# Kernel tuning notes

Hardware: AMD Instinct MI355X
Metric: run time of the kernel (lower is better)

## Reference

```python
import jax, jax.numpy as jnp
import numpy as np
from jax import lax

EPS = 1e-5

def setup_inputs() -> dict:
    key = jax.random.key(0)
    ks = jax.random.split(key, 8)
    B, D, H, W = 2, 96, 96, 96
    K, N, R = 4, 16, 6
    return {
        "x": jax.random.normal(ks[0], (B, D, H, W), jnp.float32),
        "x_proj_weight": jax.random.normal(ks[1], (K, R + 2 * N, D), jnp.float32) * 0.05,
        "dt_projs_weight": jax.random.normal(ks[2], (K, D, R), jnp.float32) * 0.05,
        "dt_projs_bias": jax.random.normal(ks[3], (K, D), jnp.float32) * 0.05,
        "A_logs": jax.random.uniform(ks[4], (K * D, N), jnp.float32, 0.0, 1.0),
        "Ds": jax.random.normal(ks[5], (K * D,), jnp.float32) * 0.1,
        "norm_weight": jnp.ones((D,), jnp.float32),
        "norm_bias": jnp.zeros((D,), jnp.float32),
    }

def _cross_scan(x):
    # x: [B,C,H,W] -> xs: [B,4,C,L]; dirs: row-major, col-major, and their flips
    B, C, H, W = x.shape
    x_hw = x.reshape(B, C, H * W)
    x_wh = jnp.swapaxes(x, 2, 3).reshape(B, C, H * W)
    return jnp.stack([x_hw, x_wh, x_hw[..., ::-1], x_wh[..., ::-1]], axis=1)

def _cross_merge(ys, H, W):
    # ys: [B,4,C,L] -> y: [B,C,L]
    B, K, C, L = ys.shape
    ys = ys[:, 0:2] + ys[:, 2:4][..., ::-1]
    y_wh = jnp.swapaxes(ys[:, 1].reshape(B, C, W, H), 2, 3).reshape(B, C, L)
    return ys[:, 0] + y_wh

def _forward(x, x_proj_weight, dt_projs_weight, dt_projs_bias, A_logs, Ds,
             norm_weight, norm_bias):
    B, D, H, W = x.shape
    L = H * W
    K, _, R = dt_projs_weight.shape
    N = A_logs.shape[1]

    xs = _cross_scan(x)                                        # [B,K,D,L]
    x_dbl = jnp.einsum('bkdl,kcd->bkcl', xs, x_proj_weight)    # [B,K,R+2N,L]
    dts, Bs, Cs = x_dbl[:, :, :R], x_dbl[:, :, R:R + N], x_dbl[:, :, R + N:]
    dts = jnp.einsum('bkrl,kdr->bkdl', dts, dt_projs_weight)   # [B,K,D,L]

    A = -jnp.exp(A_logs).reshape(K, D, N)                      # [K,D,N]
    delta = jax.nn.softplus(dts + dt_projs_bias[None, :, :, None])  # [B,K,D,L]

    # time-major for scan
    u_t = jnp.moveaxis(xs, 3, 0)       # [L,B,K,D]
    d_t = jnp.moveaxis(delta, 3, 0)    # [L,B,K,D]
    B_t = jnp.moveaxis(Bs, 3, 0)       # [L,B,K,N]
    C_t = jnp.moveaxis(Cs, 3, 0)       # [L,B,K,N]

    def step(h, inp):
        u, dlt, b, c = inp
        h = jnp.exp(dlt[..., None] * A) * h + (dlt * u)[..., None] * b[:, :, None, :]
        y = jnp.einsum('bkdn,bkn->bkd', h, c)
        return h, y

    h0 = jnp.zeros((B, K, D, N), xs.dtype)
    _, ys = lax.scan(step, h0, (u_t, d_t, B_t, C_t))           # ys: [L,B,K,D]
    ys = jnp.moveaxis(ys, 0, 3)                                # [B,K,D,L]
    ys = ys + Ds.reshape(1, K, D, 1) * xs                      # skip term

    y = _cross_merge(ys, H, W)                                 # [B,D,L]
    y = jnp.swapaxes(y, 1, 2)                                  # [B,L,D]
    # out_norm: LayerNorm over channel dim
    mu = y.mean(-1, keepdims=True)
    var = y.var(-1, keepdims=True)
    y = (y - mu) / jnp.sqrt(var + EPS) * norm_weight + norm_bias
    return y.reshape(B, H, W, D)

def reference(x, x_proj_weight, dt_projs_weight, dt_projs_bias, A_logs, Ds,
              norm_weight, norm_bias):
    return _forward(x, x_proj_weight, dt_projs_weight, dt_projs_bias,
                    A_logs, Ds, norm_weight, norm_bias)
```

## Files before the change

### kernel.cpp

```cpp
#include <hip/hip_runtime.h>
#include <hip/hip_bf16.h>
#include <hip/hip_fp16.h>


constexpr int Bn = 2, Kn = 4, Dn = 96, Hn = 96, Wn = 96, Ln = Hn * Wn;
constexpr int Nn = 16, Rn = 6;
constexpr int CCn = 192, CLn = 48;

#define DI __device__ __forceinline__

DI float bf2f(unsigned short u) { return __uint_as_float(((unsigned)u) << 16); }
DI bool probe_bf16(const void* nw) { return ((const unsigned*)nw)[0] == 0x3F803F80u; }
DI float ld_in(const void* p, long i, bool bf) {
  return bf ? bf2f(((const unsigned short*)p)[i]) : ((const float*)p)[i];
}
DI float fexp2(float x) {
#if __has_builtin(__builtin_amdgcn_exp2f)
  return __builtin_amdgcn_exp2f(x);
#else
  return exp2f(x);
#endif
}
DI float softplus_fast(float v) {
  return (v > 15.f) ? v : __logf(1.f + __expf(v));
}
constexpr float LOG2E = 1.44269504088896340736f;

__global__ __launch_bounds__(256) void k_convert(
    const void* __restrict__ xpw, const void* __restrict__ dtw,
    const void* __restrict__ dtb, const void* __restrict__ Al,
    const void* __restrict__ Ds, const void* __restrict__ nw,
    const void* __restrict__ nb,
    float* __restrict__ wp_f, float* __restrict__ wdt_f,
    float* __restrict__ bias_f, float* __restrict__ Al_f,
    float* __restrict__ dsum, float* __restrict__ nw_f, float* __restrict__ nb_f) {
  bool bf = probe_bf16(nw);
  int gtid = blockIdx.x * 256 + threadIdx.x;
  int gs = gridDim.x * 256;
  for (int i = gtid; i < Kn * 38 * Dn; i += gs) wp_f[i] = ld_in(xpw, i, bf);
  for (int i = gtid; i < Kn * Dn * Rn; i += gs) wdt_f[i] = ld_in(dtw, i, bf);
  for (int i = gtid; i < Kn * Dn; i += gs) bias_f[i] = ld_in(dtb, i, bf);
  for (int i = gtid; i < Kn * Dn * Nn; i += gs)
    Al_f[i] = -__expf(ld_in(Al, i, bf)) * LOG2E;
  for (int i = gtid; i < Dn; i += gs) {
    dsum[i] = ld_in(Ds, i, bf) + ld_in(Ds, 96 + i, bf) +
              ld_in(Ds, 192 + i, bf) + ld_in(Ds, 288 + i, bf);
    nw_f[i] = ld_in(nw, i, bf);
    nb_f[i] = ld_in(nb, i, bf);
  }
}

__global__ __launch_bounds__(256) void k_xl(const void* __restrict__ x,
                                            const void* __restrict__ nwraw,
                                            float* __restrict__ xl) {
  __shared__ float tile[96 * 97];
  bool bf = probe_bf16(nwraw);
  int l0 = blockIdx.x * 96, b = blockIdx.y;
  long srcbase = (long)b * Dn * Ln;
  for (int i = threadIdx.x; i < 96 * 96; i += 256) {
    int d = i / 96, j = i - d * 96;
    tile[d * 97 + j] = ld_in(x, srcbase + (long)d * Ln + l0 + j, bf);
  }
  __syncthreads();
  float* dst = xl + ((size_t)b * Ln + l0) * 96;
  for (int i = threadIdx.x; i < 96 * 96; i += 256) {
    int j = i / 96, d = i - j * 96;
    dst[(size_t)j * 96 + d] = tile[d * 97 + j];
  }
}

__global__ __launch_bounds__(256) void k_perm(const float* __restrict__ xl,
                                              float* __restrict__ xlT) {
  int m0 = blockIdx.x * 96, b = blockIdx.y;
  int w = blockIdx.x;
  const float* src = xl + (size_t)b * Ln * 96;
  float* dst = xlT + (size_t)b * Ln * 96;
  for (int i = threadIdx.x; i < 96 * 24; i += 256) {
    int r = i / 24, q = i - r * 24;
    *(float4*)(dst + (size_t)(m0 + r) * 96 + q * 4) =
        *(const float4*)(src + (size_t)(r * 96 + w) * 96 + q * 4);
  }
}

__global__ __launch_bounds__(256) void k_proj(
    const float* __restrict__ xl, const float* __restrict__ xlT,
    const float* __restrict__ wp_f, const float* __restrict__ wdt_f,
    const float* __restrict__ bias_f,
    __half2* __restrict__ ddu, float* __restrict__ BCg) {
  constexpr int TL = 64;
  __shared__ __half xt[TL * 102];
  __shared__ float wp[40 * 100];
  __shared__ float xd[40 * 70];
  __shared__ float wdt[96 * 6];
  __shared__ float bias[96];
  int tile = blockIdx.x, k = blockIdx.y, b = blockIdx.z;
  int l0 = tile * TL;
  int tid = threadIdx.x;
  bool rev = (k & 2) != 0;

  for (int i = tid; i < 40 * 100; i += 256) {
    int c = i / 100, dd = i - c * 100;
    wp[i] = (c < 38 && dd < 96) ? wp_f[k * 38 * 96 + c * 96 + dd] : 0.f;
  }
  for (int i = tid; i < 96 * 6; i += 256) wdt[i] = wdt_f[k * 96 * 6 + i];
  if (tid < 96) bias[tid] = bias_f[k * 96 + tid];
  {
    const float* xsrc = ((k & 1) ? xlT : xl) + (size_t)b * Ln * 96;
    for (int i = tid; i < TL * 24; i += 256) {
      int r = i / 24, q = i - r * 24;
      int g = rev ? (Ln - 1 - l0 - r) : (l0 + r);
      float4 v = *(const float4*)(xsrc + (size_t)g * 96 + q * 4);
      *(__half2*)(&xt[r * 102 + q * 4]) = __floats2half2_rn(v.x, v.y);
      *(__half2*)(&xt[r * 102 + q * 4 + 2]) = __floats2half2_rn(v.z, v.w);
    }
  }
  __syncthreads();

  {
    int jg = tid & 31, cg = tid >> 5;
    int j0 = jg * 2, c0 = cg * 5;
    float acc[5][2];
#pragma unroll
    for (int i = 0; i < 5; ++i) { acc[i][0] = 0.f; acc[i][1] = 0.f; }
    for (int dd = 0; dd < 96; dd += 4) {
      float xv[2][4];
#pragma unroll
      for (int e = 0; e < 2; ++e) {
        float2 f01 = __half22float2(*(const __half2*)&xt[(j0 + e) * 102 + dd]);
        float2 f23 = __half22float2(*(const __half2*)&xt[(j0 + e) * 102 + dd + 2]);
        xv[e][0] = f01.x; xv[e][1] = f01.y; xv[e][2] = f23.x; xv[e][3] = f23.y;
      }
#pragma unroll
      for (int i = 0; i < 5; ++i) {
        float4 w4 = *(const float4*)(wp + (c0 + i) * 100 + dd);
        const float* w = (const float*)&w4;
#pragma unroll
        for (int q = 0; q < 4; ++q) {
          acc[i][0] = fmaf(xv[0][q], w[q], acc[i][0]);
          acc[i][1] = fmaf(xv[1][q], w[q], acc[i][1]);
        }
      }
    }
#pragma unroll
    for (int i = 0; i < 5; ++i)
      *(float2*)(xd + (c0 + i) * 70 + j0) = make_float2(acc[i][0], acc[i][1]);
  }
  __syncthreads();

  size_t bk = (size_t)b * 4 + k;
  {
    float* o = BCg + (bk * (size_t)Ln + l0) * 32;
    for (int i = tid; i < TL * 32; i += 256) {
      int j = i >> 5, c = i & 31;
      o[i] = xd[(6 + c) * 70 + j];
    }
  }
  {
    int lp = tid >> 2, q = tid & 3, d0 = q * 24;
    float xr[6];
#pragma unroll
    for (int r = 0; r < 6; ++r) xr[r] = xd[r * 70 + lp];
    __half2* orow = ddu + (bk * (size_t)Ln + l0 + lp) * 96 + d0;
#pragma unroll
    for (int ii = 0; ii < 6; ++ii) {
      union { uint4 u4; __half2 h2[4]; } pk;
#pragma unroll
      for (int p = 0; p < 4; ++p) {
        int d = d0 + ii * 4 + p;
        float v = bias[d];
#pragma unroll
        for (int r = 0; r < 6; ++r) v = fmaf(xr[r], wdt[d * 6 + r], v);
        float sp = softplus_fast(v);
        float u = __half2float(xt[lp * 102 + d]);
        pk.h2[p] = __floats2half2_rn(sp, sp * u);
      }
      *(uint4*)(orow + ii * 4) = pk.u4;
    }
  }
}

DI void stage_chunk(int tid, int bk, int t0, const __half2* __restrict__ ddu,
                    const float* __restrict__ BCg, __half2* dd_s, float* bc_s) {
  const uint4* dsrc = (const uint4*)(ddu + ((size_t)bk * Ln + t0) * 96);
  uint4* ddst = (uint4*)dd_s;
  for (int i = tid; i < CLn * 96 / 4; i += 384) ddst[i] = dsrc[i];
  const float4* bsrc = (const float4*)(BCg + ((size_t)bk * Ln + t0) * 32);
  float4* bdst = (float4*)bc_s;
  for (int i = tid; i < CLn * 32 / 4; i += 384) bdst[i] = bsrc[i];
}

__global__ __launch_bounds__(384) void k_scan1(
    const __half2* __restrict__ ddu, const float* __restrict__ BCg,
    const float* __restrict__ Al_f, float* __restrict__ PSg) {
  __shared__ __half2 dd_s[CLn * 96];
  __shared__ float bc_s[CLn * 32];
  int chunk = blockIdx.x, k = blockIdx.y, b = blockIdx.z;
  int tid = threadIdx.x;
  int d = tid >> 2, ng = tid & 3, n0 = ng * 4;
  int bk = b * 4 + k;
  int bkd = bk * 96 + d;
  int t0 = chunk * CLn;
  float ac[4];
#pragma unroll
  for (int j = 0; j < 4; ++j) ac[j] = Al_f[(k * 96 + d) * 16 + n0 + j];
  stage_chunk(tid, bk, t0, ddu, BCg, dd_s, bc_s);
  __syncthreads();

  float P[4] = {1.f, 1.f, 1.f, 1.f}, S[4] = {0.f, 0.f, 0.f, 0.f};
#pragma unroll 4
  for (int t = 0; t < CLn; ++t) {
    float2 f = __half22float2(dd_s[t * 96 + d]);
    float4 Bv = *(const float4*)&bc_s[t * 32 + n0];
    const float* Ba = (const float*)&Bv;
#pragma unroll
    for (int j = 0; j < 4; ++j) {
      float a = fexp2(f.x * ac[j]);
      P[j] *= a;
      S[j] = fmaf(a, S[j], f.y * Ba[j]);
    }
  }
  size_t ob = ((size_t)bkd * CCn + chunk) * 32 + n0;
  *(float4*)(PSg + ob) = make_float4(P[0], P[1], P[2], P[3]);
  *(float4*)(PSg + ob + 16) = make_float4(S[0], S[1], S[2], S[3]);
}

__global__ __launch_bounds__(256) void k_midscan(float* __restrict__ PSg) {
  __shared__ float Pl[256], Sl[256];
  int bkd = blockIdx.x;
  int tid = threadIdx.x;
  int g = tid >> 4, n = tid & 15;
  constexpr int CPG = CCn / 16;
  size_t base = ((size_t)bkd * CCn + (size_t)g * CPG) * 32 + n;
  float Pr[CPG], Sr[CPG];
#pragma unroll
  for (int i = 0; i < CPG; ++i) {
    Pr[i] = PSg[base + (size_t)i * 32];
    Sr[i] = PSg[base + (size_t)i * 32 + 16];
  }
  float Pa = 1.f, Sa = 0.f;
#pragma unroll
  for (int i = 0; i < CPG; ++i) { Sa = fmaf(Pr[i], Sa, Sr[i]); Pa *= Pr[i]; }
  Pl[tid] = Pa;
  Sl[tid] = Sa;
  __syncthreads();
#pragma unroll
  for (int s = 1; s < 16; s <<= 1) {
    float Pp = 1.f, Sp = 0.f;
    if (g >= s) { Pp = Pl[(g - s) * 16 + n]; Sp = Sl[(g - s) * 16 + n]; }
    __syncthreads();
    if (g >= s) {
      Sl[tid] = fmaf(Pl[tid], Sp, Sl[tid]);
      Pl[tid] *= Pp;
    }
    __syncthreads();
  }
  float h = (g == 0) ? 0.f : Sl[(g - 1) * 16 + n];
#pragma unroll
  for (int i = 0; i < CPG; ++i) {
    PSg[base + (size_t)i * 32] = h;
    h = fmaf(Pr[i], h, Sr[i]);
  }
}

__global__ __launch_bounds__(384) void k_scan2(
    const __half2* __restrict__ ddu, const float* __restrict__ BCg,
    const float* __restrict__ Al_f, const float* __restrict__ PSg,
    float* __restrict__ ysS) {
  __shared__ __half2 dd_s[CLn * 96];
  __shared__ float bc_s[CLn * 32];
  int chunk = blockIdx.x, k = blockIdx.y, b = blockIdx.z;
  int tid = threadIdx.x;
  int d = tid >> 2, ng = tid & 3, n0 = ng * 4;
  int bk = b * 4 + k;
  int bkd = bk * 96 + d;
  int t0 = chunk * CLn;
  float ac[4];
#pragma unroll
  for (int j = 0; j < 4; ++j) ac[j] = Al_f[(k * 96 + d) * 16 + n0 + j];
  stage_chunk(tid, bk, t0, ddu, BCg, dd_s, bc_s);
  float4 h4 = *(const float4*)(PSg + ((size_t)bkd * CCn + chunk) * 32 + n0);
  float h[4] = {h4.x, h4.y, h4.z, h4.w};
  __syncthreads();

#pragma unroll 4
  for (int t = 0; t < CLn; ++t) {
    float2 f = __half22float2(dd_s[t * 96 + d]);
    float4 Bv = *(const float4*)&bc_s[t * 32 + n0];
    float4 Cv = *(const float4*)&bc_s[t * 32 + 16 + n0];
    const float* Ba = (const float*)&Bv;
    const float* Ca = (const float*)&Cv;
    float py = 0.f;
#pragma unroll
    for (int j = 0; j < 4; ++j) {
      float a = fexp2(f.x * ac[j]);
      h[j] = fmaf(a, h[j], f.y * Ba[j]);
      py = fmaf(h[j], Ca[j], py);
    }
    py += __shfl_xor(py, 1);
    py += __shfl_xor(py, 2);
    if (ng == 0) ysS[((size_t)bk * Ln + t0 + t) * 96 + d] = py;
  }
}

__global__ __launch_bounds__(256) void k_merge_ln(
    const float* __restrict__ ysS, const float* __restrict__ xl,
    const float* __restrict__ dsum, const void* __restrict__ nwraw,
    const float* __restrict__ nw_f, const float* __restrict__ nb_f,
    void* __restrict__ outv) {
  __shared__ float yt[64 * 97];
  __shared__ float nwf[96], nbf[96], mu_s[64], rs_s[64];
  bool bf = probe_bf16(nwraw);
  int tile = blockIdx.x, b = blockIdx.y;
  int h0 = (tile / 12) * 8, w0 = (tile % 12) * 8;
  int tid = threadIdx.x;
  if (tid < 96) { nwf[tid] = nw_f[tid]; nbf[tid] = nb_f[tid]; }
  const float* y0 = ysS + (size_t)(b * 4 + 0) * Ln * 96;
  const float* y1 = ysS + (size_t)(b * 4 + 1) * Ln * 96;
  const float* y2 = ysS + (size_t)(b * 4 + 2) * Ln * 96;
  const float* y3 = ysS + (size_t)(b * 4 + 3) * Ln * 96;
  const float* xb = xl + (size_t)b * Ln * 96;
  for (int i = tid; i < 64 * 96; i += 256) {
    int rr = i / 96, d = i - rr * 96;
    int hh = h0 + (rr >> 3), ww = w0 + (rr & 7);
    int l = hh * 96 + ww, t1 = ww * 96 + hh;
    float v = y0[(size_t)l * 96 + d] + y1[(size_t)t1 * 96 + d] +
              y2[(size_t)(Ln - 1 - l) * 96 + d] +
              y3[(size_t)(Ln - 1 - t1) * 96 + d] +
              dsum[d] * xb[(size_t)l * 96 + d];
    yt[rr * 97 + d] = v;
  }
  __syncthreads();
  if (tid < 64) {
    float s = 0.f, ss = 0.f;
#pragma unroll 4
    for (int d = 0; d < 96; ++d) {
      float v = yt[tid * 97 + d];
      s += v;
      ss += v * v;
    }
    float mu = s * (1.f / 96.f);
    float var = fmaxf(ss * (1.f / 96.f) - mu * mu, 0.f);
    mu_s[tid] = mu;
    rs_s[tid] = rsqrtf(var + 1e-5f);
  }
  __syncthreads();
  for (int i = tid; i < 64 * 96; i += 256) {
    int rr = i / 96, d = i - rr * 96;
    int hh = h0 + (rr >> 3), ww = w0 + (rr & 7);
    size_t idx = ((size_t)b * Ln + hh * 96 + ww) * 96 + d;
    float v = (yt[rr * 97 + d] - mu_s[rr]) * rs_s[rr] * nwf[d] + nbf[d];
    if (bf) ((__hip_bfloat16*)outv)[idx] = __float2bfloat16(v);
    else    ((float*)outv)[idx] = v;
  }
}

extern "C" void kernel_launch(void* const* d_in, const int* in_sizes, int n_in,
                              void* d_out, int out_size, void* d_ws, size_t ws_size,
                              hipStream_t stream) {
  const void* x   = d_in[0];
  const void* xpw = d_in[1];
  const void* dtw = d_in[2];
  const void* dtb = d_in[3];
  const void* Al  = d_in[4];
  const void* Ds  = d_in[5];
  const void* nw  = d_in[6];
  const void* nb  = d_in[7];

  char* ws = (char*)d_ws;
  size_t off = 0;
  auto alloc = [&](size_t bytes) {
    char* p = ws + off;
    off += (bytes + 511) & ~(size_t)511;
    return p;
  };
  float* xl    = (float*)alloc((size_t)Bn * Ln * Dn * 4);
  float* xlT   = (float*)alloc((size_t)Bn * Ln * Dn * 4);
  float* wp_f  = (float*)alloc((size_t)Kn * 38 * Dn * 4);
  float* wdt_f = (float*)alloc((size_t)Kn * Dn * Rn * 4);
  float* bias_f= (float*)alloc((size_t)Kn * Dn * 4);
  float* Al_f  = (float*)alloc((size_t)Kn * Dn * Nn * 4);
  float* dsum  = (float*)alloc((size_t)Dn * 4);
  float* nw_f  = (float*)alloc((size_t)Dn * 4);
  float* nb_f  = (float*)alloc((size_t)Dn * 4);
  __half2* ddu = (__half2*)alloc((size_t)Bn * Kn * Ln * Dn * 4);
  float* BC    = (float*)alloc((size_t)Bn * Kn * Ln * 32 * 4);
  float* PS    = (float*)alloc((size_t)Bn * Kn * Dn * CCn * 32 * 4);
  float* ysS   = (float*)alloc((size_t)Bn * Kn * Ln * Dn * 4);
  (void)ws_size; (void)in_sizes; (void)n_in; (void)out_size;

  k_convert<<<dim3(64), dim3(256), 0, stream>>>(xpw, dtw, dtb, Al, Ds, nw, nb,
                                                wp_f, wdt_f, bias_f, Al_f,
                                                dsum, nw_f, nb_f);
  k_xl<<<dim3(Ln / 96, Bn), dim3(256), 0, stream>>>(x, nw, xl);
  k_perm<<<dim3(Ln / 96, Bn), dim3(256), 0, stream>>>(xl, xlT);
  k_proj<<<dim3(Ln / 64, Kn, Bn), dim3(256), 0, stream>>>(xl, xlT, wp_f, wdt_f,
                                                          bias_f, ddu, BC);
  k_scan1<<<dim3(CCn, Kn, Bn), dim3(384), 0, stream>>>(ddu, BC, Al_f, PS);
  k_midscan<<<dim3(Bn * Kn * Dn), dim3(256), 0, stream>>>(PS);
  k_scan2<<<dim3(CCn, Kn, Bn), dim3(384), 0, stream>>>(ddu, BC, Al_f, PS, ysS);
  k_merge_ln<<<dim3(144, Bn), dim3(256), 0, stream>>>(ysS, xl, dsum, nw, nw_f,
                                                      nb_f, d_out);
}
```

Baseline: 201.0 us.

## Store B/C and scan outputs in fp16; fuse transpose and permute kernels

Merges the x transpose kernel and the row/column permute kernel into one kernel that writes both xl and xlT from a single shared tile, dropping one launch and a full re-read of xl. The B/C projection buffer and the per-direction scan outputs are now stored as fp16 instead of fp32, roughly halving the bytes moved between k_proj, the two scan kernels and the merge/LayerNorm kernel. scan1 stages only the B half of the buffer into shared memory. The trade-off is reduced precision in B, C and the partial outputs before the final merge and normalisation.

```diff
diff --git a/kernel.cpp b/kernel.cpp
--- a/kernel.cpp
+++ b/kernel.cpp
@@ -50,35 +50,26 @@
   }
 }
 
-__global__ __launch_bounds__(256) void k_xl(const void* __restrict__ x,
-                                            const void* __restrict__ nwraw,
-                                            float* __restrict__ xl) {
+__global__ __launch_bounds__(256) void k_prep(const void* __restrict__ x,
+                                              const void* __restrict__ nwraw,
+                                              float* __restrict__ xl,
+                                              float* __restrict__ xlT) {
   __shared__ float tile[96 * 97];
   bool bf = probe_bf16(nwraw);
-  int l0 = blockIdx.x * 96, b = blockIdx.y;
-  long srcbase = (long)b * Dn * Ln;
+  int h = blockIdx.x, b = blockIdx.y;
+  long srcbase = (long)b * Dn * Ln + (long)h * 96;
   for (int i = threadIdx.x; i < 96 * 96; i += 256) {
-    int d = i / 96, j = i - d * 96;
-    tile[d * 97 + j] = ld_in(x, srcbase + (long)d * Ln + l0 + j, bf);
-  }
-  __syncthreads();
-  float* dst = xl + ((size_t)b * Ln + l0) * 96;
+    int d = i / 96, w = i - d * 96;
+    tile[d * 97 + w] = ld_in(x, srcbase + (long)d * Ln + w, bf);
+  }
+  __syncthreads();
+  float* xlb = xl + (size_t)b * Ln * 96;
+  float* xTb = xlT + (size_t)b * Ln * 96;
   for (int i = threadIdx.x; i < 96 * 96; i += 256) {
-    int j = i / 96, d = i - j * 96;
-    dst[(size_t)j * 96 + d] = tile[d * 97 + j];
-  }
-}
-
-__global__ __launch_bounds__(256) void k_perm(const float* __restrict__ xl,
-                                              float* __restrict__ xlT) {
-  int m0 = blockIdx.x * 96, b = blockIdx.y;
-  int w = blockIdx.x;
-  const float* src = xl + (size_t)b * Ln * 96;
-  float* dst = xlT + (size_t)b * Ln * 96;
-  for (int i = threadIdx.x; i < 96 * 24; i += 256) {
-    int r = i / 24, q = i - r * 24;
-    *(float4*)(dst + (size_t)(m0 + r) * 96 + q * 4) =
-        *(const float4*)(src + (size_t)(r * 96 + w) * 96 + q * 4);
+    int w = i / 96, d = i - w * 96;
+    float v = tile[d * 97 + w];
+    xlb[(size_t)(h * 96 + w) * 96 + d] = v;
+    xTb[(size_t)(w * 96 + h) * 96 + d] = v;
   }
 }
 
@@ -86,7 +77,7 @@
     const float* __restrict__ xl, const float* __restrict__ xlT,
     const float* __restrict__ wp_f, const float* __restrict__ wdt_f,
     const float* __restrict__ bias_f,
-    __half2* __restrict__ ddu, float* __restrict__ BCg) {
+    __half2* __restrict__ ddu, __half* __restrict__ BCh) {
   constexpr int TL = 64;
   __shared__ __half xt[TL * 102];
   __shared__ float wp[40 * 100];
@@ -149,10 +140,10 @@
 
   size_t bk = (size_t)b * 4 + k;
   {
-    float* o = BCg + (bk * (size_t)Ln + l0) * 32;
+    __half* o = BCh + (bk * (size_t)Ln + l0) * 32;
     for (int i = tid; i < TL * 32; i += 256) {
       int j = i >> 5, c = i & 31;
-      o[i] = xd[(6 + c) * 70 + j];
+      o[i] = __float2half(xd[(6 + c) * 70 + j]);
     }
   }
   {
@@ -179,21 +170,11 @@
   }
 }
 
-DI void stage_chunk(int tid, int bk, int t0, const __half2* __restrict__ ddu,
-                    const float* __restrict__ BCg, __half2* dd_s, float* bc_s) {
-  const uint4* dsrc = (const uint4*)(ddu + ((size_t)bk * Ln + t0) * 96);
-  uint4* ddst = (uint4*)dd_s;
-  for (int i = tid; i < CLn * 96 / 4; i += 384) ddst[i] = dsrc[i];
-  const float4* bsrc = (const float4*)(BCg + ((size_t)bk * Ln + t0) * 32);
-  float4* bdst = (float4*)bc_s;
-  for (int i = tid; i < CLn * 32 / 4; i += 384) bdst[i] = bsrc[i];
-}
-
 __global__ __launch_bounds__(384) void k_scan1(
-    const __half2* __restrict__ ddu, const float* __restrict__ BCg,
+    const __half2* __restrict__ ddu, const __half* __restrict__ BCh,
     const float* __restrict__ Al_f, float* __restrict__ PSg) {
   __shared__ __half2 dd_s[CLn * 96];
-  __shared__ float bc_s[CLn * 32];
+  __shared__ __half b_s[CLn * 16];
   int chunk = blockIdx.x, k = blockIdx.y, b = blockIdx.z;
   int tid = threadIdx.x;
   int d = tid >> 2, ng = tid & 3, n0 = ng * 4;
@@ -203,15 +184,28 @@
   float ac[4];
 #pragma unroll
   for (int j = 0; j < 4; ++j) ac[j] = Al_f[(k * 96 + d) * 16 + n0 + j];
-  stage_chunk(tid, bk, t0, ddu, BCg, dd_s, bc_s);
+  {
+    const uint4* dsrc = (const uint4*)(ddu + ((size_t)bk * Ln + t0) * 96);
+    uint4* ddst = (uint4*)dd_s;
+    for (int i = tid; i < CLn * 96 / 4; i += 384) ddst[i] = dsrc[i];
+    const unsigned* bsrc = (const unsigned*)(BCh + ((size_t)bk * Ln + t0) * 32);
+    unsigned* bdst = (unsigned*)b_s;
+    for (int i = tid; i < CLn * 8; i += 384) {
+      int t = i >> 3, q = i & 7;
+      bdst[t * 8 + q] = bsrc[t * 16 + q];
+    }
+  }
   __syncthreads();
 
   float P[4] = {1.f, 1.f, 1.f, 1.f}, S[4] = {0.f, 0.f, 0.f, 0.f};
 #pragma unroll 4
   for (int t = 0; t < CLn; ++t) {
     float2 f = __half22float2(dd_s[t * 96 + d]);
-    float4 Bv = *(const float4*)&bc_s[t * 32 + n0];
-    const float* Ba = (const float*)&Bv;
+    union { uint2 u; __half2 h2[2]; } bv;
+    bv.u = *(const uint2*)&b_s[t * 16 + n0];
+    float2 b01 = __half22float2(bv.h2[0]);
+    float2 b23 = __half22float2(bv.h2[1]);
+    float Ba[4] = {b01.x, b01.y, b23.x, b23.y};
 #pragma unroll
     for (int j = 0; j < 4; ++j) {
       float a = fexp2(f.x * ac[j]);
@@ -263,11 +257,11 @@
 }
 
 __global__ __launch_bounds__(384) void k_scan2(
-    const __half2* __restrict__ ddu, const float* __restrict__ BCg,
+    const __half2* __restrict__ ddu, const __half* __restrict__ BCh,
     const float* __restrict__ Al_f, const float* __restrict__ PSg,
-    float* __restrict__ ysS) {
+    __half* __restrict__ ysH) {
   __shared__ __half2 dd_s[CLn * 96];
-  __shared__ float bc_s[CLn * 32];
+  __shared__ __half bc_s[CLn * 32];
   int chunk = blockIdx.x, k = blockIdx.y, b = blockIdx.z;
   int tid = threadIdx.x;
   int d = tid >> 2, ng = tid & 3, n0 = ng * 4;
@@ -277,7 +271,14 @@
   float ac[4];
 #pragma unroll
   for (int j = 0; j < 4; ++j) ac[j] = Al_f[(k * 96 + d) * 16 + n0 + j];
-  stage_chunk(tid, bk, t0, ddu, BCg, dd_s, bc_s);
+  {
+    const uint4* dsrc = (const uint4*)(ddu + ((size_t)bk * Ln + t0) * 96);
+    uint4* ddst = (uint4*)dd_s;
+    for (int i = tid; i < CLn * 96 / 4; i += 384) ddst[i] = dsrc[i];
+    const uint4* bsrc = (const uint4*)(BCh + ((size_t)bk * Ln + t0) * 32);
+    uint4* bdst = (uint4*)bc_s;
+    for (int i = tid; i < CLn * 32 * 2 / 16; i += 384) bdst[i] = bsrc[i];
+  }
   float4 h4 = *(const float4*)(PSg + ((size_t)bkd * CCn + chunk) * 32 + n0);
   float h[4] = {h4.x, h4.y, h4.z, h4.w};
   __syncthreads();
@@ -285,10 +286,15 @@
 #pragma unroll 4
   for (int t = 0; t < CLn; ++t) {
     float2 f = __half22float2(dd_s[t * 96 + d]);
-    float4 Bv = *(const float4*)&bc_s[t * 32 + n0];
-    float4 Cv = *(const float4*)&bc_s[t * 32 + 16 + n0];
-    const float* Ba = (const float*)&Bv;
-    const float* Ca = (const float*)&Cv;
+    union { uint2 u; __half2 h2[2]; } bv, cv;
+    bv.u = *(const uint2*)&bc_s[t * 32 + n0];
+    cv.u = *(const uint2*)&bc_s[t * 32 + 16 + n0];
+    float2 b01 = __half22float2(bv.h2[0]);
+    float2 b23 = __half22float2(bv.h2[1]);
+    float2 c01 = __half22float2(cv.h2[0]);
+    float2 c23 = __half22float2(cv.h2[1]);
+    float Ba[4] = {b01.x, b01.y, b23.x, b23.y};
+    float Ca[4] = {c01.x, c01.y, c23.x, c23.y};
     float py = 0.f;
 #pragma unroll
     for (int j = 0; j < 4; ++j) {
@@ -298,12 +304,12 @@
     }
     py += __shfl_xor(py, 1);
     py += __shfl_xor(py, 2);
-    if (ng == 0) ysS[((size_t)bk * Ln + t0 + t) * 96 + d] = py;
+    if (ng == 0) ysH[((size_t)bk * Ln + t0 + t) * 96 + d] = __float2half(py);
   }
 }
 
 __global__ __launch_bounds__(256) void k_merge_ln(
-    const float* __restrict__ ysS, const float* __restrict__ xl,
+    const __half* __restrict__ ysH, const float* __restrict__ xl,
     const float* __restrict__ dsum, const void* __restrict__ nwraw,
     const float* __restrict__ nw_f, const float* __restrict__ nb_f,
     void* __restrict__ outv) {
@@ -314,18 +320,19 @@
   int h0 = (tile / 12) * 8, w0 = (tile % 12) * 8;
   int tid = threadIdx.x;
   if (tid < 96) { nwf[tid] = nw_f[tid]; nbf[tid] = nb_f[tid]; }
-  const float* y0 = ysS + (size_t)(b * 4 + 0) * Ln * 96;
-  const float* y1 = ysS + (size_t)(b * 4 + 1) * Ln * 96;
-  const float* y2 = ysS + (size_t)(b * 4 + 2) * Ln * 96;
-  const float* y3 = ysS + (size_t)(b * 4 + 3) * Ln * 96;
+  const __half* y0 = ysH + (size_t)(b * 4 + 0) * Ln * 96;
+  const __half* y1 = ysH + (size_t)(b * 4 + 1) * Ln * 96;
+  const __half* y2 = ysH + (size_t)(b * 4 + 2) * Ln * 96;
+  const __half* y3 = ysH + (size_t)(b * 4 + 3) * Ln * 96;
   const float* xb = xl + (size_t)b * Ln * 96;
   for (int i = tid; i < 64 * 96; i += 256) {
     int rr = i / 96, d = i - rr * 96;
     int hh = h0 + (rr >> 3), ww = w0 + (rr & 7);
     int l = hh * 96 + ww, t1 = ww * 96 + hh;
-    float v = y0[(size_t)l * 96 + d] + y1[(size_t)t1 * 96 + d] +
-              y2[(size_t)(Ln - 1 - l) * 96 + d] +
-              y3[(size_t)(Ln - 1 - t1) * 96 + d] +
+    float v = __half2float(y0[(size_t)l * 96 + d]) +
+              __half2float(y1[(size_t)t1 * 96 + d]) +
+              __half2float(y2[(size_t)(Ln - 1 - l) * 96 + d]) +
+              __half2float(y3[(size_t)(Ln - 1 - t1) * 96 + d]) +
               dsum[d] * xb[(size_t)l * 96 + d];
     yt[rr * 97 + d] = v;
   }
@@ -383,21 +390,20 @@
   float* nw_f  = (float*)alloc((size_t)Dn * 4);
   float* nb_f  = (float*)alloc((size_t)Dn * 4);
   __half2* ddu = (__half2*)alloc((size_t)Bn * Kn * Ln * Dn * 4);
-  float* BC    = (float*)alloc((size_t)Bn * Kn * Ln * 32 * 4);
+  __half* BCh  = (__half*)alloc((size_t)Bn * Kn * Ln * 32 * 2);
   float* PS    = (float*)alloc((size_t)Bn * Kn * Dn * CCn * 32 * 4);
-  float* ysS   = (float*)alloc((size_t)Bn * Kn * Ln * Dn * 4);
+  __half* ysH  = (__half*)alloc((size_t)Bn * Kn * Ln * Dn * 2);
   (void)ws_size; (void)in_sizes; (void)n_in; (void)out_size;
 
   k_convert<<<dim3(64), dim3(256), 0, stream>>>(xpw, dtw, dtb, Al, Ds, nw, nb,
                                                 wp_f, wdt_f, bias_f, Al_f,
                                                 dsum, nw_f, nb_f);
-  k_xl<<<dim3(Ln / 96, Bn), dim3(256), 0, stream>>>(x, nw, xl);
-  k_perm<<<dim3(Ln / 96, Bn), dim3(256), 0, stream>>>(xl, xlT);
+  k_prep<<<dim3(Hn, Bn), dim3(256), 0, stream>>>(x, nw, xl, xlT);
   k_proj<<<dim3(Ln / 64, Kn, Bn), dim3(256), 0, stream>>>(xl, xlT, wp_f, wdt_f,
-                                                          bias_f, ddu, BC);
-  k_scan1<<<dim3(CCn, Kn, Bn), dim3(384), 0, stream>>>(ddu, BC, Al_f, PS);
+                                                          bias_f, ddu, BCh);
+  k_scan1<<<dim3(CCn, Kn, Bn), dim3(384), 0, stream>>>(ddu, BCh, Al_f, PS);
   k_midscan<<<dim3(Bn * Kn * Dn), dim3(256), 0, stream>>>(PS);
-  k_scan2<<<dim3(CCn, Kn, Bn), dim3(384), 0, stream>>>(ddu, BC, Al_f, PS, ysS);
-  k_merge_ln<<<dim3(144, Bn), dim3(256), 0, stream>>>(ysS, xl, dsum, nw, nw_f,
+  k_scan2<<<dim3(CCn, Kn, Bn), dim3(384), 0, stream>>>(ddu, BCh, Al_f, PS, ysH);
+  k_merge_ln<<<dim3(144, Bn), dim3(256), 0, stream>>>(ysH, xl, dsum, nw, nw_f,
                                                       nb_f, d_out);
 }
```

After: 203.7 us. About the same (+1.4%).
